# Performance work log

Measured on AMD Instinct MI355X. Metric: run time of the kernel, lower is better.

The kernel has to match this reference:

```python
import jax, jax.numpy as jnp
import numpy as np

EMB_NUM = 1024
EMB_DIM = 256


def setup_inputs() -> dict:
    key = jax.random.key(0)
    k1, k2 = jax.random.split(key)
    z = jax.random.normal(k1, (64, 32, 32, EMB_DIM), dtype=jnp.float32)
    # nn.Embedding weight initialized uniform(-1/emb_num, 1/emb_num)
    emb = jax.random.uniform(k2, (EMB_NUM, EMB_DIM), dtype=jnp.float32,
                             minval=-1.0 / EMB_NUM, maxval=1.0 / EMB_NUM)
    return {"z": z, "emb": emb}


def reference(z, emb):
    z_shape = z.shape
    flat_z = z.reshape(-1, EMB_DIM)                      # [N, D]
    # squared-distance matrix: ||z||^2 + ||e||^2 - 2 z.e  -> [N, K]
    distance = (jnp.sum(flat_z ** 2, axis=1, keepdims=True)
                + jnp.sum(emb ** 2, axis=1)
                - 2.0 * jnp.matmul(flat_z, emb.T))
    idx = jnp.argmin(distance, axis=1)                   # [N]
    # one-hot @ emb is just a gather of the nearest codebook rows
    quantized_z = jnp.take(emb, idx, axis=0).reshape(z_shape)
    commitment_loss = 0.5 * jnp.mean((jax.lax.stop_gradient(quantized_z) - z) ** 2)
    emb_loss = 0.5 * jnp.mean((quantized_z - jax.lax.stop_gradient(z)) ** 2)
    # straight-through estimator
    quantized_z = z + jax.lax.stop_gradient(quantized_z - z)
    return (quantized_z, commitment_loss, emb_loss)
```

## Files before the change

kernel.cpp:

```cpp
#include <hip/hip_runtime.h>

#define K_CODES 1024
#define DIM     256
#define NROWS   65536
#define THREADS 256
#define ROWS_PER_WAVE 32
#define ROWS_PER_BLOCK 128
#define NBLOCKS (NROWS / ROWS_PER_BLOCK)
#define NCHUNK  64

typedef __attribute__((ext_vector_type(8))) short short8;
typedef __attribute__((ext_vector_type(4))) float f32x4;

__device__ __forceinline__ unsigned short f2bf(float f) {
    unsigned int u = __float_as_uint(f);
    u += 0x7fffu + ((u >> 16) & 1u);
    return (unsigned short)(u >> 16);
}

__global__ void k_prep(const float* __restrict__ emb,
                       unsigned short* __restrict__ embb2,
                       float* __restrict__ hneT,
                       float* __restrict__ lossAcc) {
    __shared__ float snormw[8][16];
    const int c   = blockIdx.x;
    const int tid = threadIdx.x;
    const int m   = tid >> 6;
    const int l   = tid & 63;
    const int r   = l & 15;
    const int q   = l >> 4;

    const float* src = emb + (size_t)(c * 16 + r) * DIM + m * 32 + q * 8;
    float4 a = *reinterpret_cast<const float4*>(src);
    float4 b = *reinterpret_cast<const float4*>(src + 4);
    float s = a.x*a.x + a.y*a.y + a.z*a.z + a.w*a.w
            + b.x*b.x + b.y*b.y + b.z*b.z + b.w*b.w;
    short8 sv;
    sv[0]=(short)f2bf(a.x); sv[1]=(short)f2bf(a.y); sv[2]=(short)f2bf(a.z); sv[3]=(short)f2bf(a.w);
    sv[4]=(short)f2bf(b.x); sv[5]=(short)f2bf(b.y); sv[6]=(short)f2bf(b.z); sv[7]=(short)f2bf(b.w);
    reinterpret_cast<short8*>(embb2)[(size_t)(c * 8 + m) * 64 + l] = sv;

    s += __shfl_xor(s, 16, 64);
    s += __shfl_xor(s, 32, 64);
    if (l < 16) snormw[m][l] = s;
    __syncthreads();
    if (tid < 16) {
        float t = 0.f;
        #pragma unroll
        for (int mm = 0; mm < 8; ++mm) t += snormw[mm][tid];
        hneT[c * 16 + tid] = -0.5f * t;
    }
    if (c == 0 && tid == 0) *lossAcc = 0.f;
}

__launch_bounds__(THREADS, 2)
__global__ void k_main(const float* __restrict__ z,
                       const unsigned short* __restrict__ embb2,
                       const float* __restrict__ hneT,
                       const float* __restrict__ emb,
                       float* __restrict__ out,
                       float* __restrict__ lossAcc) {
    const int tid  = threadIdx.x;
    const int lane = tid & 63;
    const int w    = tid >> 6;
    const int r    = lane & 15;
    const int q    = lane >> 4;
    const long grow0 = (long)blockIdx.x * ROWS_PER_BLOCK + w * ROWS_PER_WAVE;

    short8 af[2][8];
    float  zn[2];
    #pragma unroll
    for (int t = 0; t < 2; ++t) {
        const float* zr = z + (grow0 + t * 16 + r) * DIM + q * 8;
        float s = 0.f;
        #pragma unroll
        for (int m = 0; m < 8; ++m) {
            float4 a = *reinterpret_cast<const float4*>(zr + m * 32);
            float4 b = *reinterpret_cast<const float4*>(zr + m * 32 + 4);
            s += a.x*a.x + a.y*a.y + a.z*a.z + a.w*a.w
               + b.x*b.x + b.y*b.y + b.z*b.z + b.w*b.w;
            short8 sv;
            sv[0]=(short)f2bf(a.x); sv[1]=(short)f2bf(a.y); sv[2]=(short)f2bf(a.z); sv[3]=(short)f2bf(a.w);
            sv[4]=(short)f2bf(b.x); sv[5]=(short)f2bf(b.y); sv[6]=(short)f2bf(b.z); sv[7]=(short)f2bf(b.w);
            af[t][m] = sv;
        }
        s += __shfl_xor(s, 16, 64);
        s += __shfl_xor(s, 32, 64);
        zn[t] = s;
    }

    float kb0[4], kb1[4];
    #pragma unroll
    for (int j = 0; j < 4; ++j) { kb0[j] = -1e30f; kb1[j] = -1e30f; }

    const char* ebase = reinterpret_cast<const char*>(embb2) + (size_t)lane * 16;

    auto loadc = [&](short8 (&buf)[8], int c) {
        const char* bp = ebase + (size_t)c * 8192;
        #pragma unroll
        for (int m = 0; m < 8; ++m)
            buf[m] = *reinterpret_cast<const short8*>(bp + m * 1024);
    };
    auto compute = [&](short8 (&buf)[8], int c) {
        const float hne = hneT[c * 16 + r];
        f32x4 a0 = {hne, hne, hne, hne};
        f32x4 a1 = {hne, hne, hne, hne};
        #pragma unroll
        for (int m = 0; m < 8; ++m) {
            a0 = __builtin_amdgcn_mfma_f32_16x16x32_bf16(af[0][m], buf[m], a0, 0, 0, 0);
            a1 = __builtin_amdgcn_mfma_f32_16x16x32_bf16(af[1][m], buf[m], a1, 0, 0, 0);
        }
        const unsigned tag = 1023u - (unsigned)(c * 16 + r);
        #pragma unroll
        for (int j = 0; j < 4; ++j) {
            kb0[j] = fmaxf(kb0[j], __uint_as_float((__float_as_uint(a0[j]) & 0xFFFFFC00u) | tag));
            kb1[j] = fmaxf(kb1[j], __uint_as_float((__float_as_uint(a1[j]) & 0xFFFFFC00u) | tag));
        }
    };

    short8 bufA[8], bufB[8];
    loadc(bufA, 0);
    for (int c = 0; c < NCHUNK; c += 2) {
        loadc(bufB, c + 1);
        compute(bufA, c);
        if (c + 2 < NCHUNK) loadc(bufA, c + 2);
        compute(bufB, c + 1);
    }

    #pragma unroll
    for (int j = 0; j < 4; ++j) {
        #pragma unroll
        for (int m = 1; m < 16; m <<= 1) {
            kb0[j] = fmaxf(kb0[j], __shfl_xor(kb0[j], m, 64));
            kb1[j] = fmaxf(kb1[j], __shfl_xor(kb1[j], m, 64));
        }
    }

    float lp = 0.f;
    #pragma unroll
    for (int rr = 0; rr < 32; ++rr) {
        const int t = rr >> 4, r16 = rr & 15;
        const int qq = r16 >> 2, rsub = r16 & 3;
        float kv = __shfl((t == 0) ? kb0[rsub] : kb1[rsub], qq * 16, 64);
        const unsigned ku = __float_as_uint(kv);
        const int   code  = 1023 - (int)(ku & 1023u);
        const float score = __uint_as_float(ku & 0xFFFFFC00u);
        float4 v = *reinterpret_cast<const float4*>(emb + (size_t)code * DIM + lane * 4);
        *reinterpret_cast<float4*>(out + (size_t)(grow0 + rr) * DIM + lane * 4) = v;
        float zr = __shfl(zn[t], r16, 64);
        lp += zr - 2.f * score;
    }
    if (lane == 0) atomicAdd(lossAcc, lp);
}

__global__ void k_loss(const float* __restrict__ lossAcc, float* __restrict__ out2) {
    float loss = 0.5f * lossAcc[0] * (1.f / 16777216.f);
    out2[0] = loss;
    out2[1] = loss;
}

extern "C" void kernel_launch(void* const* d_in, const int* in_sizes, int n_in,
                              void* d_out, int out_size, void* d_ws, size_t ws_size,
                              hipStream_t stream) {
    const float* z   = (const float*)d_in[0];
    const float* emb = (const float*)d_in[1];
    float* out = (float*)d_out;
    char*  ws  = (char*)d_ws;
    float* lossAcc        = (float*)ws;
    float* hneT           = (float*)(ws + 256);
    unsigned short* embb2 = (unsigned short*)(ws + 256 + 4096);

    k_prep<<<K_CODES / 16, 512, 0, stream>>>(emb, embb2, hneT, lossAcc);
    k_main<<<NBLOCKS, THREADS, 0, stream>>>(z, embb2, hneT, emb, out, lossAcc);
    k_loss<<<1, 1, 0, stream>>>(lossAcc, out + (long)NROWS * DIM);
}
```

Baseline: 167.2 us.

## Split codebook search across two waves per row tile with shared-memory argmax merge

```diff
diff --git a/kernel.cpp b/kernel.cpp
--- a/kernel.cpp
+++ b/kernel.cpp
@@ -3,11 +3,10 @@
 #define K_CODES 1024
 #define DIM     256
 #define NROWS   65536
-#define THREADS 256
-#define ROWS_PER_WAVE 32
-#define ROWS_PER_BLOCK 128
+#define THREADS 128
+#define ROWS_PER_BLOCK 32
 #define NBLOCKS (NROWS / ROWS_PER_BLOCK)
-#define NCHUNK  64
+#define CHUNKS_PER_WAVE 32
 
 typedef __attribute__((ext_vector_type(8))) short short8;
 typedef __attribute__((ext_vector_type(4))) float f32x4;
@@ -53,19 +52,22 @@
     if (c == 0 && tid == 0) *lossAcc = 0.f;
 }
 
-__launch_bounds__(THREADS, 2)
+__launch_bounds__(THREADS, 4)
 __global__ void k_main(const float* __restrict__ z,
                        const unsigned short* __restrict__ embb2,
                        const float* __restrict__ hneT,
                        const float* __restrict__ emb,
                        float* __restrict__ out,
                        float* __restrict__ lossAcc) {
+    __shared__ float skey[2][32];
+    __shared__ float szn[32];
+
     const int tid  = threadIdx.x;
     const int lane = tid & 63;
     const int w    = tid >> 6;
     const int r    = lane & 15;
     const int q    = lane >> 4;
-    const long grow0 = (long)blockIdx.x * ROWS_PER_BLOCK + w * ROWS_PER_WAVE;
+    const long grow0 = (long)blockIdx.x * ROWS_PER_BLOCK;
 
     short8 af[2][8];
     float  zn[2];
@@ -88,12 +90,15 @@
         s += __shfl_xor(s, 32, 64);
         zn[t] = s;
     }
+    if (w == 0 && lane < 16) { szn[lane] = zn[0]; szn[16 + lane] = zn[1]; }
 
     float kb0[4], kb1[4];
     #pragma unroll
     for (int j = 0; j < 4; ++j) { kb0[j] = -1e30f; kb1[j] = -1e30f; }
 
-    const char* ebase = reinterpret_cast<const char*>(embb2) + (size_t)lane * 16;
+    const int c0 = w * CHUNKS_PER_WAVE;
+    const char* ebase = reinterpret_cast<const char*>(embb2)
+                        + (size_t)c0 * 8192 + (size_t)lane * 16;
 
     auto loadc = [&](short8 (&buf)[8], int c) {
         const char* bp = ebase + (size_t)c * 8192;
@@ -102,7 +107,8 @@
             buf[m] = *reinterpret_cast<const short8*>(bp + m * 1024);
     };
     auto compute = [&](short8 (&buf)[8], int c) {
-        const float hne = hneT[c * 16 + r];
+        const int gcode = (c0 + c) * 16 + r;
+        const float hne = hneT[gcode];
         f32x4 a0 = {hne, hne, hne, hne};
         f32x4 a1 = {hne, hne, hne, hne};
         #pragma unroll
@@ -110,7 +116,7 @@
             a0 = __builtin_amdgcn_mfma_f32_16x16x32_bf16(af[0][m], buf[m], a0, 0, 0, 0);
             a1 = __builtin_amdgcn_mfma_f32_16x16x32_bf16(af[1][m], buf[m], a1, 0, 0, 0);
         }
-        const unsigned tag = 1023u - (unsigned)(c * 16 + r);
+        const unsigned tag = 1023u - (unsigned)gcode;
         #pragma unroll
         for (int j = 0; j < 4; ++j) {
             kb0[j] = fmaxf(kb0[j], __uint_as_float((__float_as_uint(a0[j]) & 0xFFFFFC00u) | tag));
@@ -120,10 +126,10 @@
 
     short8 bufA[8], bufB[8];
     loadc(bufA, 0);
-    for (int c = 0; c < NCHUNK; c += 2) {
+    for (int c = 0; c < CHUNKS_PER_WAVE; c += 2) {
         loadc(bufB, c + 1);
         compute(bufA, c);
-        if (c + 2 < NCHUNK) loadc(bufA, c + 2);
+        if (c + 2 < CHUNKS_PER_WAVE) loadc(bufA, c + 2);
         compute(bufB, c + 1);
     }
 
@@ -136,21 +142,36 @@
         }
     }
 
-    float lp = 0.f;
     #pragma unroll
     for (int rr = 0; rr < 32; ++rr) {
         const int t = rr >> 4, r16 = rr & 15;
         const int qq = r16 >> 2, rsub = r16 & 3;
-        float kv = __shfl((t == 0) ? kb0[rsub] : kb1[rsub], qq * 16, 64);
+        const float kv = (t == 0) ? kb0[rsub] : kb1[rsub];
+        if (lane == qq * 16) skey[w][rr] = kv;
+    }
+    __syncthreads();
+
+    #pragma unroll
+    for (int i = 0; i < 16; ++i) {
+        const int rr = i * 2 + w;
+        const float kv = fmaxf(skey[0][rr], skey[1][rr]);
         const unsigned ku = __float_as_uint(kv);
-        const int   code  = 1023 - (int)(ku & 1023u);
-        const float score = __uint_as_float(ku & 0xFFFFFC00u);
+        const int code = 1023 - (int)(ku & 1023u);
         float4 v = *reinterpret_cast<const float4*>(emb + (size_t)code * DIM + lane * 4);
         *reinterpret_cast<float4*>(out + (size_t)(grow0 + rr) * DIM + lane * 4) = v;
-        float zr = __shfl(zn[t], r16, 64);
-        lp += zr - 2.f * score;
     }
-    if (lane == 0) atomicAdd(lossAcc, lp);
+
+    if (w == 0) {
+        float lp = 0.f;
+        if (lane < 32) {
+            const float kv = fmaxf(skey[0][lane], skey[1][lane]);
+            const float score = __uint_as_float(__float_as_uint(kv) & 0xFFFFFC00u);
+            lp = szn[lane] - 2.f * score;
+        }
+        #pragma unroll
+        for (int m = 1; m < 64; m <<= 1) lp += __shfl_xor(lp, m, 64);
+        if (lane == 0) atomicAdd(lossAcc, lp);
+    }
 }
 
 __global__ void k_loss(const float* __restrict__ lossAcc, float* __restrict__ out2) {
```

New measurement: 427.0 us. 155% more time.

## Stage codebook chunks in LDS via async global_load_lds double buffering

Applied to the files above, without the earlier changes.

```diff
diff --git a/kernel.cpp b/kernel.cpp
--- a/kernel.cpp
+++ b/kernel.cpp
@@ -7,7 +7,9 @@
 #define ROWS_PER_WAVE 32
 #define ROWS_PER_BLOCK 128
 #define NBLOCKS (NROWS / ROWS_PER_BLOCK)
-#define NCHUNK  64
+#define CHUNK_CODES 32
+#define NCHUNK (K_CODES / CHUNK_CODES)
+#define CHUNK_BYTES (CHUNK_CODES * DIM * 2)
 
 typedef __attribute__((ext_vector_type(8))) short short8;
 typedef __attribute__((ext_vector_type(4))) float f32x4;
@@ -16,6 +18,12 @@
     unsigned int u = __float_as_uint(f);
     u += 0x7fffu + ((u >> 16) & 1u);
     return (unsigned short)(u >> 16);
+}
+
+__device__ __forceinline__ void gload_lds16(const void* g, void* l) {
+    __builtin_amdgcn_global_load_lds(
+        (const __attribute__((address_space(1))) void*)g,
+        (__attribute__((address_space(3))) void*)l, 16, 0, 0);
 }
 
 __global__ void k_prep(const float* __restrict__ emb,
@@ -60,12 +68,22 @@
                        const float* __restrict__ emb,
                        float* __restrict__ out,
                        float* __restrict__ lossAcc) {
+    __shared__ __align__(16) char ebuf[2][CHUNK_BYTES];
+
     const int tid  = threadIdx.x;
     const int lane = tid & 63;
     const int w    = tid >> 6;
     const int r    = lane & 15;
     const int q    = lane >> 4;
     const long grow0 = (long)blockIdx.x * ROWS_PER_BLOCK + w * ROWS_PER_WAVE;
+
+    {
+        const char* src = reinterpret_cast<const char*>(embb2) + (size_t)tid * 16;
+        char* dst = ebuf[0] + tid * 16;
+        #pragma unroll
+        for (int j = 0; j < 4; ++j)
+            gload_lds16(src + j * 4096, dst + j * 4096);
+    }
 
     short8 af[2][8];
     float  zn[2];
@@ -93,38 +111,45 @@
     #pragma unroll
     for (int j = 0; j < 4; ++j) { kb0[j] = -1e30f; kb1[j] = -1e30f; }
 
-    const char* ebase = reinterpret_cast<const char*>(embb2) + (size_t)lane * 16;
-
-    auto loadc = [&](short8 (&buf)[8], int c) {
-        const char* bp = ebase + (size_t)c * 8192;
-        #pragma unroll
-        for (int m = 0; m < 8; ++m)
-            buf[m] = *reinterpret_cast<const short8*>(bp + m * 1024);
-    };
-    auto compute = [&](short8 (&buf)[8], int c) {
-        const float hne = hneT[c * 16 + r];
-        f32x4 a0 = {hne, hne, hne, hne};
-        f32x4 a1 = {hne, hne, hne, hne};
-        #pragma unroll
-        for (int m = 0; m < 8; ++m) {
-            a0 = __builtin_amdgcn_mfma_f32_16x16x32_bf16(af[0][m], buf[m], a0, 0, 0, 0);
-            a1 = __builtin_amdgcn_mfma_f32_16x16x32_bf16(af[1][m], buf[m], a1, 0, 0, 0);
-        }
-        const unsigned tag = 1023u - (unsigned)(c * 16 + r);
-        #pragma unroll
-        for (int j = 0; j < 4; ++j) {
-            kb0[j] = fmaxf(kb0[j], __uint_as_float((__float_as_uint(a0[j]) & 0xFFFFFC00u) | tag));
-            kb1[j] = fmaxf(kb1[j], __uint_as_float((__float_as_uint(a1[j]) & 0xFFFFFC00u) | tag));
-        }
-    };
-
-    short8 bufA[8], bufB[8];
-    loadc(bufA, 0);
-    for (int c = 0; c < NCHUNK; c += 2) {
-        loadc(bufB, c + 1);
-        compute(bufA, c);
-        if (c + 2 < NCHUNK) loadc(bufA, c + 2);
-        compute(bufB, c + 1);
+    __syncthreads();
+
+    for (int c = 0; c < NCHUNK; ++c) {
+        const int cur = c & 1;
+        if (c + 1 < NCHUNK) {
+            const char* src = reinterpret_cast<const char*>(embb2)
+                              + (size_t)(c + 1) * CHUNK_BYTES + (size_t)tid * 16;
+            char* dst = ebuf[cur ^ 1] + tid * 16;
+            #pragma unroll
+            for (int j = 0; j < 4; ++j)
+                gload_lds16(src + j * 4096, dst + j * 4096);
+        }
+
+        const float hne0 = hneT[c * CHUNK_CODES + r];
+        const float hne1 = hneT[c * CHUNK_CODES + 16 + r];
+        const char* bbase = ebuf[cur] + (size_t)lane * 16;
+
+        #pragma unroll
+        for (int g = 0; g < 2; ++g) {
+            short8 bf[8];
+            #pragma unroll
+            for (int m = 0; m < 8; ++m)
+                bf[m] = *reinterpret_cast<const short8*>(bbase + (g * 8 + m) * 1024);
+            const float hne = (g == 0) ? hne0 : hne1;
+            f32x4 a0 = {hne, hne, hne, hne};
+            f32x4 a1 = {hne, hne, hne, hne};
+            #pragma unroll
+            for (int m = 0; m < 8; ++m) {
+                a0 = __builtin_amdgcn_mfma_f32_16x16x32_bf16(af[0][m], bf[m], a0, 0, 0, 0);
+                a1 = __builtin_amdgcn_mfma_f32_16x16x32_bf16(af[1][m], bf[m], a1, 0, 0, 0);
+            }
+            const unsigned tag = 1023u - (unsigned)(c * CHUNK_CODES + g * 16 + r);
+            #pragma unroll
+            for (int j = 0; j < 4; ++j) {
+                kb0[j] = fmaxf(kb0[j], __uint_as_float((__float_as_uint(a0[j]) & 0xFFFFFC00u) | tag));
+                kb1[j] = fmaxf(kb1[j], __uint_as_float((__float_as_uint(a1[j]) & 0xFFFFFC00u) | tag));
+            }
+        }
+        __syncthreads();
     }
 
     #pragma unroll
```

Result: faster. 163.4 us (-2.3%).
